# Kernel tuning notes

Hardware: AMD Instinct MI355X
Metric: run time of the kernel (lower is better)

Reference implementation:

```python
import jax, jax.numpy as jnp
import numpy as np

E = 1024        # embedding_dim
H = 16          # n_heads
DK = 64         # qk_dim
DV = 64         # v_dim
P = 512         # projection_dim (latent kv bottleneck)
BASE = 10000.0


def rope(x):
    # x: [B, H, S, D] with D even; interleaved (even/odd) RoPE rotation
    S, D = x.shape[-2], x.shape[-1]
    theta = BASE ** (-2.0 * jnp.arange(D // 2, dtype=x.dtype) / D)      # [D/2]
    ang = jnp.arange(S, dtype=x.dtype)[:, None] * theta[None, :]        # [S, D/2]
    cos, sin = jnp.cos(ang), jnp.sin(ang)
    x1, x2 = x[..., ::2], x[..., 1::2]                                  # [B,H,S,D/2]
    out = jnp.stack([x1 * cos - x2 * sin, x1 * sin + x2 * cos], axis=-1)
    return out.reshape(x.shape)


def setup_inputs() -> dict:
    key = jax.random.key(0)
    ks = jax.random.split(key, 10)
    s = lambda fan_in: 1.0 / np.sqrt(fan_in)
    x = jax.random.normal(ks[0], (2, 2048, E), dtype=jnp.float32)
    Wq = jax.random.uniform(ks[1], (E, DK * H), jnp.float32, -s(E), s(E))
    bq = jax.random.uniform(ks[2], (DK * H,), jnp.float32, -s(E), s(E))
    Wkv1 = jax.random.uniform(ks[3], (E, P), jnp.float32, -s(E), s(E))
    bkv1 = jax.random.uniform(ks[4], (P,), jnp.float32, -s(E), s(E))
    Wkv2 = jax.random.uniform(ks[5], (P, (DK + DV) * H), jnp.float32, -s(P), s(P))
    bkv2 = jax.random.uniform(ks[6], ((DK + DV) * H,), jnp.float32, -s(P), s(P))
    Wo = jax.random.uniform(ks[7], (H * DV, E), jnp.float32, -s(H * DV), s(H * DV))
    bo = jax.random.uniform(ks[8], (E,), jnp.float32, -s(H * DV), s(H * DV))
    return {"x": x, "Wq": Wq, "bq": bq, "Wkv1": Wkv1, "bkv1": bkv1,
            "Wkv2": Wkv2, "bkv2": bkv2, "Wo": Wo, "bo": bo}


def reference(x, Wq, bq, Wkv1, bkv1, Wkv2, bkv2, Wo, bo):
    B, S, _ = x.shape  # seq == max_context, so truncation x[:, -max_context:] is a no-op
    q = x @ Wq + bq                                            # [B,S,H*DK]
    kv = (x @ Wkv1 + bkv1) @ Wkv2 + bkv2                       # [B,S,(DK+DV)*H]
    k, v = kv[..., : DK * H], kv[..., DK * H:]
    q = q.reshape(B, S, H, DK).transpose(0, 2, 1, 3)           # [B,H,S,DK]
    k = k.reshape(B, S, H, DK).transpose(0, 2, 1, 3)
    v = v.reshape(B, S, H, DV).transpose(0, 2, 1, 3)           # [B,H,S,DV]
    q = rope(q)
    k = rope(k)
    scores = jnp.einsum('bhqd,bhkd->bhqk', q, k) * (1.0 / np.sqrt(DK))
    causal = jnp.tril(jnp.ones((S, S), dtype=bool))
    scores = jnp.where(causal, scores, -jnp.inf)
    probs = jax.nn.softmax(scores, axis=-1)                    # dropout skipped (eval)
    attn = jnp.einsum('bhqk,bhkd->bhqd', probs, v)             # [B,H,S,DV]
    attn = attn.transpose(0, 2, 1, 3).reshape(B, S, H * DV)
    return attn @ Wo + bo                                      # [B,S,E]
```

## Files before the change

### kernel.cpp

```cpp
#include <hip/hip_runtime.h>
#include <hip/hip_bf16.h>
#include <stdint.h>
#include <math.h>

#define S_ 2048
#define H_ 16
#define B_ 2

typedef __attribute__((ext_vector_type(4))) float f32x4;
typedef __attribute__((ext_vector_type(8))) short s16x8;

static __device__ __forceinline__ uint16_t f2bf(float f) {
    union { float f; uint32_t u; } x; x.f = f;
    uint32_t u = x.u;
    return (uint16_t)((u + 0x7FFFu + ((u >> 16) & 1u)) >> 16);
}

static __device__ __forceinline__ void gl_lds16(const uint16_t* g, uint16_t* l) {
    __builtin_amdgcn_global_load_lds(
        (const __attribute__((address_space(1))) unsigned int*)g,
        (__attribute__((address_space(3))) unsigned int*)l, 16, 0, 0);
}


__global__ void cvt_f32_bf16(const float* __restrict__ in, uint16_t* __restrict__ out, int n4) {
    int i = blockIdx.x * blockDim.x + threadIdx.x;
    if (i >= n4) return;
    float4 v = ((const float4*)in)[i];
    union { uint16_t h[4]; uint64_t q; } pk;
    pk.h[0] = f2bf(v.x); pk.h[1] = f2bf(v.y); pk.h[2] = f2bf(v.z); pk.h[3] = f2bf(v.w);
    ((uint64_t*)out)[i] = pk.q;
}

__global__ void transpose_w(const float* __restrict__ in, uint16_t* __restrict__ out, int R, int C) {
    __shared__ float sm[32][33];
    int r0 = blockIdx.x * 32, c0 = blockIdx.y * 32;
    int t = threadIdx.x;
    int rr = t >> 3, cc = (t & 7) * 4;
    float4 v = *(const float4*)(in + (size_t)(r0 + rr) * C + c0 + cc);
    sm[rr][cc] = v.x; sm[rr][cc + 1] = v.y; sm[rr][cc + 2] = v.z; sm[rr][cc + 3] = v.w;
    __syncthreads();
    union { uint16_t h[4]; uint64_t q; } pk;
    #pragma unroll
    for (int i = 0; i < 4; i++) pk.h[i] = f2bf(sm[cc + i][rr]);
    *(uint64_t*)(out + (size_t)(c0 + rr) * R + r0 + cc) = pk.q;
}

__global__ void rope_table(float* __restrict__ cosT, float* __restrict__ sinT) {
    int i = blockIdx.x * blockDim.x + threadIdx.x;
    int s = i >> 5, j = i & 31;
    float theta = powf(10000.0f, -2.0f * (float)j / 64.0f);
    float ang = (float)s * theta;
    cosT[i] = cosf(ang);
    sinT[i] = sinf(ang);
}

__global__ void vtrans(const uint16_t* __restrict__ vb, uint16_t* __restrict__ vt) {
    __shared__ __align__(16) uint16_t sm[64][72];
    int s0 = blockIdx.x * 64;
    int bh = blockIdx.y;
    const uint16_t* src = vb + (size_t)bh * S_ * 64;
    uint16_t* dst = vt + (size_t)bh * 64 * S_;
    int t = threadIdx.x;
    #pragma unroll
    for (int p = 0; p < 2; p++) {
        int off = p * 2048 + t * 8;
        int sl = off >> 6, d = off & 63;
        s16x8 v = *(const s16x8*)(src + (size_t)(s0 + sl) * 64 + d);
        #pragma unroll
        for (int i = 0; i < 8; i++) sm[sl][d + i] = (uint16_t)v[i];
    }
    __syncthreads();
    #pragma unroll
    for (int p = 0; p < 2; p++) {
        int off = p * 2048 + t * 8;
        int d = off >> 6, sl = off & 63;
        union { uint16_t h[8]; s16x8 v; } pk;
        #pragma unroll
        for (int i = 0; i < 8; i++) pk.h[i] = sm[sl + i][d];
        *(s16x8*)(dst + (size_t)d * S_ + s0 + sl) = pk.v;
    }
}


#define MODE_F32   0
#define MODE_BF16  1
#define MODE_QROPE 2
#define MODE_KV    3

#define QSCALE 0.180336880f

template<int MODE>
__global__ __launch_bounds__(256, 2)
void gemm_bt(const uint16_t* __restrict__ A, const uint16_t* __restrict__ BT,
             const float* __restrict__ bias,
             void* __restrict__ out0, uint16_t* __restrict__ out2,
             const float* __restrict__ cosT, const float* __restrict__ sinT,
             int N, int K)
{
    __shared__ __align__(16) uint16_t smA[128 * 32];
    __shared__ __align__(16) uint16_t smB[128 * 32];
    const int t = threadIdx.x;
    const int l = t & 63;
    const int wid = t >> 6;
    const int wr = wid >> 1, wc = wid & 1;
    const int m0 = blockIdx.x * 128, n0 = blockIdx.y * 128;

    f32x4 acc[4][4];
    #pragma unroll
    for (int i = 0; i < 4; i++)
        #pragma unroll
        for (int j = 0; j < 4; j++) acc[i][j] = (f32x4)(0.0f);

    const int srow = t >> 2;
    const int ssw = (((t & 3) ^ (srow & 3)) * 8);
    const uint16_t* aG = A + (size_t)(m0 + srow) * K + ssw;
    const uint16_t* bG = BT + (size_t)(n0 + srow) * K + ssw;
    uint16_t* lA = smA + t * 8;
    uint16_t* lB = smB + t * 8;

    const int rchunk = (((l >> 4) ^ (l & 3)) * 8);

    for (int k0 = 0; k0 < K; k0 += 32) {
        __syncthreads();
        gl_lds16(aG + k0, lA);
        gl_lds16(aG + (size_t)64 * K + k0, lA + 2048);
        gl_lds16(bG + k0, lB);
        gl_lds16(bG + (size_t)64 * K + k0, lB + 2048);
        __syncthreads();
        s16x8 af[4], bfr[4];
        #pragma unroll
        for (int mf = 0; mf < 4; mf++)
            af[mf] = *(const s16x8*)(smA + (wr * 64 + mf * 16 + (l & 15)) * 32 + rchunk);
        #pragma unroll
        for (int nf = 0; nf < 4; nf++)
            bfr[nf] = *(const s16x8*)(smB + (wc * 64 + nf * 16 + (l & 15)) * 32 + rchunk);
        #pragma unroll
        for (int mf = 0; mf < 4; mf++)
            #pragma unroll
            for (int nf = 0; nf < 4; nf++)
                acc[mf][nf] = __builtin_amdgcn_mfma_f32_16x16x32_bf16(af[mf], bfr[nf], acc[mf][nf], 0, 0, 0);
    }

    const int rbase = m0 + wr * 64 + ((l >> 4) << 2);
    const int cbase = n0 + wc * 64 + (l & 15);
    #pragma unroll
    for (int mf = 0; mf < 4; mf++) {
        #pragma unroll
        for (int nf = 0; nf < 4; nf++) {
            const int col = cbase + nf * 16;
            const float bv = bias[col];
            #pragma unroll
            for (int r = 0; r < 4; r++) {
                const int row = rbase + mf * 16 + r;
                float v = acc[mf][nf][r] + bv;
                if constexpr (MODE == MODE_F32) {
                    ((float*)out0)[(size_t)row * N + col] = v;
                } else if constexpr (MODE == MODE_BF16) {
                    ((uint16_t*)out0)[(size_t)row * N + col] = f2bf(v);
                } else {
                    float other = __shfl_xor(v, 1);
                    int s = row & (S_ - 1);
                    int b = row >> 11;
                    if constexpr (MODE == MODE_QROPE) {
                        int h = col >> 6, d = col & 63;
                        float c = cosT[s * 32 + (d >> 1)];
                        float sn = sinT[s * 32 + (d >> 1)];
                        float o = (d & 1) ? (other * sn + v * c) : (v * c - other * sn);
                        o *= QSCALE;
                        ((uint16_t*)out0)[((size_t)(b * H_ + h) * S_ + s) * 64 + d] = f2bf(o);
                    } else {
                        if (col < 1024) {
                            int h = col >> 6, d = col & 63;
                            float c = cosT[s * 32 + (d >> 1)];
                            float sn = sinT[s * 32 + (d >> 1)];
                            float o = (d & 1) ? (other * sn + v * c) : (v * c - other * sn);
                            ((uint16_t*)out0)[((size_t)(b * H_ + h) * S_ + s) * 64 + d] = f2bf(o);
                        } else {
                            int cc = col - 1024;
                            int h = cc >> 6, d = cc & 63;
                            out2[((size_t)(b * H_ + h) * S_ + s) * 64 + d] = f2bf(v);
                        }
                    }
                }
            }
        }
    }
}


__global__ __launch_bounds__(256, 4)
void attn_fa(const uint16_t* __restrict__ qr, const uint16_t* __restrict__ kr,
             const uint16_t* __restrict__ vt, uint16_t* __restrict__ attnf)
{
    __shared__ __align__(16) uint16_t smK[2][4096];
    __shared__ __align__(16) uint16_t smV[2][4096];
    __shared__ __align__(16) uint16_t smP[4096];

    const int t = threadIdx.x;
    const int l = t & 63;
    const int w = t >> 6;
    const int bh = blockIdx.y;
    const int bb = bh >> 4, hh = bh & 15;
    const uint16_t* qB = qr + (size_t)bh * S_ * 64;
    const uint16_t* kB = kr + (size_t)bh * S_ * 64;
    const uint16_t* vB = vt + (size_t)bh * 64 * S_;

    const int arow = t >> 3;
    const int asw = (((t & 7) ^ (arow & 7)) * 8);
    const int frow = l & 15;
    const int fg = l >> 4;
    const int rsw = l & 7;

    auto stage = [&](int buf, int kv0) {
        gl_lds16(kB + (size_t)(kv0 + arow) * 64 + asw, &smK[buf][t * 8]);
        gl_lds16(kB + (size_t)(kv0 + arow + 32) * 64 + asw, &smK[buf][2048 + t * 8]);
        gl_lds16(vB + (size_t)arow * S_ + kv0 + asw, &smV[buf][t * 8]);
        gl_lds16(vB + (size_t)(arow + 32) * S_ + kv0 + asw, &smV[buf][2048 + t * 8]);
    };

    auto process = [&](int qt) {
        s16x8 qf[2];
        {
            const uint16_t* qp = qB + (size_t)(qt * 64 + w * 16 + frow) * 64 + fg * 8;
            qf[0] = *(const s16x8*)qp;
            qf[1] = *(const s16x8*)(qp + 32);
        }
        float mrow[4], lrow[4];
        f32x4 oacc[4];
        #pragma unroll
        for (int r = 0; r < 4; r++) { mrow[r] = -INFINITY; lrow[r] = 0.0f; }
        #pragma unroll
        for (int nf = 0; nf < 4; nf++) oacc[nf] = (f32x4)(0.0f);

        const int nkt = qt + 1;
        int cur = 0;
        stage(0, qt ? 0 : 0);
        __syncthreads();

        for (int kt = 0; kt < nkt; kt++) {
            if (kt + 1 < nkt) stage(cur ^ 1, (kt + 1) * 64);

            f32x4 sacc[4];
            #pragma unroll
            for (int nf = 0; nf < 4; nf++) sacc[nf] = (f32x4)(0.0f);
            #pragma unroll
            for (int kk = 0; kk < 2; kk++) {
                #pragma unroll
                for (int nf = 0; nf < 4; nf++) {
                    s16x8 kf = *(const s16x8*)(&smK[cur][(nf * 16 + frow) * 64 + (((kk * 4 + fg) ^ rsw) * 8)]);
                    sacc[nf] = __builtin_amdgcn_mfma_f32_16x16x32_bf16(qf[kk], kf, sacc[nf], 0, 0, 0);
                }
            }

            const bool diag = (kt == qt);
            #pragma unroll
            for (int r = 0; r < 4; r++) {
                const int qloc = w * 16 + fg * 4 + r;
                float sv[4];
                #pragma unroll
                for (int nf = 0; nf < 4; nf++) {
                    float s = sacc[nf][r];
                    if (diag) s = (nf * 16 + frow <= qloc) ? s : -INFINITY;
                    sv[nf] = s;
                }
                float mx = fmaxf(fmaxf(sv[0], sv[1]), fmaxf(sv[2], sv[3]));
                mx = fmaxf(mx, __shfl_xor(mx, 1));
                mx = fmaxf(mx, __shfl_xor(mx, 2));
                mx = fmaxf(mx, __shfl_xor(mx, 4));
                mx = fmaxf(mx, __shfl_xor(mx, 8));
                float nm = fmaxf(mrow[r], mx);
                float fac = __builtin_amdgcn_exp2f(mrow[r] - nm);
                float ps = 0.0f;
                float pb[4];
                #pragma unroll
                for (int nf = 0; nf < 4; nf++) {
                    float p = __builtin_amdgcn_exp2f(sv[nf] - nm);
                    pb[nf] = p;
                    ps += p;
                }
                ps += __shfl_xor(ps, 1);
                ps += __shfl_xor(ps, 2);
                ps += __shfl_xor(ps, 4);
                ps += __shfl_xor(ps, 8);
                lrow[r] = lrow[r] * fac + ps;
                mrow[r] = nm;
                #pragma unroll
                for (int nf = 0; nf < 4; nf++) oacc[nf][r] *= fac;
                const int prow = w * 16 + fg * 4 + r;
                const int prm = (fg * 4 + r) & 7;
                #pragma unroll
                for (int nf = 0; nf < 4; nf++)
                    smP[prow * 64 + (((nf * 2 + (frow >> 3)) ^ prm) * 8) + (frow & 7)] = f2bf(pb[nf]);
            }

            #pragma unroll
            for (int kk = 0; kk < 2; kk++) {
                s16x8 pf = *(const s16x8*)(&smP[(w * 16 + frow) * 64 + (((kk * 4 + fg) ^ rsw) * 8)]);
                #pragma unroll
                for (int nf = 0; nf < 4; nf++) {
                    s16x8 vf = *(const s16x8*)(&smV[cur][(nf * 16 + frow) * 64 + (((kk * 4 + fg) ^ rsw) * 8)]);
                    oacc[nf] = __builtin_amdgcn_mfma_f32_16x16x32_bf16(pf, vf, oacc[nf], 0, 0, 0);
                }
            }

            __syncthreads();
            cur ^= 1;
        }

        #pragma unroll
        for (int r = 0; r < 4; r++) {
            float rinv = __builtin_amdgcn_rcpf(lrow[r]);
            const int qrow = qt * 64 + w * 16 + fg * 4 + r;
            #pragma unroll
            for (int nf = 0; nf < 4; nf++) {
                int d = nf * 16 + frow;
                attnf[((size_t)(bb * S_ + qrow)) * 1024 + hh * 64 + d] = f2bf(oacc[nf][r] * rinv);
            }
        }
    };

    const int j = blockIdx.x;
    process(j);
    process(31 - j);
}


extern "C" void kernel_launch(void* const* d_in, const int* in_sizes, int n_in,
                              void* d_out, int out_size, void* d_ws, size_t ws_size,
                              hipStream_t stream)
{
    const float* x    = (const float*)d_in[0];
    const float* Wq   = (const float*)d_in[1];
    const float* bq   = (const float*)d_in[2];
    const float* Wkv1 = (const float*)d_in[3];
    const float* bkv1 = (const float*)d_in[4];
    const float* Wkv2 = (const float*)d_in[5];
    const float* bkv2 = (const float*)d_in[6];
    const float* Wo   = (const float*)d_in[7];
    const float* bo   = (const float*)d_in[8];
    float* out = (float*)d_out;
    char* ws = (char*)d_ws;

    uint16_t* xb    = (uint16_t*)(ws + 0);
    uint16_t* WqT   = (uint16_t*)(ws + 8388608);
    uint16_t* Wkv1T = (uint16_t*)(ws + 10485760);
    uint16_t* Wkv2T = (uint16_t*)(ws + 11534336);
    uint16_t* WoT   = (uint16_t*)(ws + 13631488);
    float*    cosT  = (float*)(ws + 15728640);
    float*    sinT  = (float*)(ws + 15990784);
    uint16_t* qrb   = (uint16_t*)(ws + 16252928);
    uint16_t* kv1b  = (uint16_t*)(ws + 24641536);
    uint16_t* krb   = (uint16_t*)(ws + 28835840);
    uint16_t* vbb   = (uint16_t*)(ws + 37224448);
    uint16_t* vtb   = (uint16_t*)(ws + 45613056);
    uint16_t* attnf = (uint16_t*)(ws + 54001664);

    cvt_f32_bf16<<<4096, 256, 0, stream>>>(x, xb, 1048576);
    transpose_w<<<dim3(32, 32), 256, 0, stream>>>(Wq, WqT, 1024, 1024);
    transpose_w<<<dim3(32, 16), 256, 0, stream>>>(Wkv1, Wkv1T, 1024, 512);
    transpose_w<<<dim3(16, 64), 256, 0, stream>>>(Wkv2, Wkv2T, 512, 2048);
    transpose_w<<<dim3(32, 32), 256, 0, stream>>>(Wo, WoT, 1024, 1024);
    rope_table<<<256, 256, 0, stream>>>(cosT, sinT);

    gemm_bt<MODE_QROPE><<<dim3(32, 8), 256, 0, stream>>>(xb, WqT, bq, qrb, nullptr, cosT, sinT, 1024, 1024);
    gemm_bt<MODE_BF16><<<dim3(32, 4), 256, 0, stream>>>(xb, Wkv1T, bkv1, kv1b, nullptr, nullptr, nullptr, 512, 1024);
    gemm_bt<MODE_KV><<<dim3(32, 16), 256, 0, stream>>>(kv1b, Wkv2T, bkv2, krb, vbb, cosT, sinT, 2048, 512);
    vtrans<<<dim3(32, 32), 256, 0, stream>>>(vbb, vtb);
    attn_fa<<<dim3(16, 32), 256, 0, stream>>>(qrb, krb, vtb, attnf);
    gemm_bt<MODE_F32><<<dim3(32, 8), 256, 0, stream>>>(attnf, WoT, bo, out, nullptr, nullptr, nullptr, 1024, 1024);
}
```

Before: 275.5 us.

## Double-buffer GEMM with narrower tiles and restructure flash attention to transposed scores

The GEMM now uses 128x64 tiles with double-buffered LDS staging, one barrier per k-step and a higher occupancy target, and the launch grids are doubled to match. The attention kernel computes S^T (K as the A operand), so each lane owns a single query column and the row max and sum need only two cross-lane shuffles. P is packed with v_cvt_pk_bf16 into vector LDS stores, and one q-tile per block replaces the paired tiles. This is meant to cut barrier stalls and softmax shuffle overhead, at the risk of load imbalance across causal q-tiles and extra A reloads in the GEMM. The rope table now uses exp2f in place of powf.

```diff
diff --git a/kernel.cpp b/kernel.cpp
--- a/kernel.cpp
+++ b/kernel.cpp
@@ -14,6 +14,12 @@
     union { float f; uint32_t u; } x; x.f = f;
     uint32_t u = x.u;
     return (uint16_t)((u + 0x7FFFu + ((u >> 16) & 1u)) >> 16);
+}
+
+static __device__ __forceinline__ uint32_t cvtpk_bf16(float a, float b) {
+    uint32_t d;
+    asm("v_cvt_pk_bf16_f32 %0, %1, %2" : "=v"(d) : "v"(a), "v"(b));
+    return d;
 }
 
 static __device__ __forceinline__ void gl_lds16(const uint16_t* g, uint16_t* l) {
@@ -49,7 +55,7 @@
 __global__ void rope_table(float* __restrict__ cosT, float* __restrict__ sinT) {
     int i = blockIdx.x * blockDim.x + threadIdx.x;
     int s = i >> 5, j = i & 31;
-    float theta = powf(10000.0f, -2.0f * (float)j / 64.0f);
+    float theta = exp2f(-0.41524101f * (float)j);
     float ang = (float)s * theta;
     cosT[i] = cosf(ang);
     sinT[i] = sinf(ang);
@@ -91,63 +97,67 @@
 #define QSCALE 0.180336880f
 
 template<int MODE>
-__global__ __launch_bounds__(256, 2)
+__global__ __launch_bounds__(256, 4)
 void gemm_bt(const uint16_t* __restrict__ A, const uint16_t* __restrict__ BT,
              const float* __restrict__ bias,
              void* __restrict__ out0, uint16_t* __restrict__ out2,
              const float* __restrict__ cosT, const float* __restrict__ sinT,
              int N, int K)
 {
-    __shared__ __align__(16) uint16_t smA[128 * 32];
-    __shared__ __align__(16) uint16_t smB[128 * 32];
+    __shared__ __align__(16) uint16_t smA[2][4096];
+    __shared__ __align__(16) uint16_t smB[2][2048];
     const int t = threadIdx.x;
     const int l = t & 63;
     const int wid = t >> 6;
     const int wr = wid >> 1, wc = wid & 1;
-    const int m0 = blockIdx.x * 128, n0 = blockIdx.y * 128;
-
-    f32x4 acc[4][4];
+    const int m0 = blockIdx.x * 128, n0 = blockIdx.y * 64;
+
+    f32x4 acc[4][2];
     #pragma unroll
     for (int i = 0; i < 4; i++)
         #pragma unroll
-        for (int j = 0; j < 4; j++) acc[i][j] = (f32x4)(0.0f);
+        for (int j = 0; j < 2; j++) acc[i][j] = (f32x4)(0.0f);
 
     const int srow = t >> 2;
     const int ssw = (((t & 3) ^ (srow & 3)) * 8);
     const uint16_t* aG = A + (size_t)(m0 + srow) * K + ssw;
     const uint16_t* bG = BT + (size_t)(n0 + srow) * K + ssw;
-    uint16_t* lA = smA + t * 8;
-    uint16_t* lB = smB + t * 8;
 
     const int rchunk = (((l >> 4) ^ (l & 3)) * 8);
 
+    auto stage = [&](int buf, int k0) {
+        gl_lds16(aG + k0, &smA[buf][t * 8]);
+        gl_lds16(aG + (size_t)64 * K + k0, &smA[buf][2048 + t * 8]);
+        gl_lds16(bG + k0, &smB[buf][t * 8]);
+    };
+
+    stage(0, 0);
+    __syncthreads();
+    int cur = 0;
     for (int k0 = 0; k0 < K; k0 += 32) {
+        if (k0 + 32 < K) stage(cur ^ 1, k0 + 32);
+        s16x8 af[4], bfr[2];
+        #pragma unroll
+        for (int mf = 0; mf < 4; mf++)
+            af[mf] = *(const s16x8*)(&smA[cur][(wr * 64 + mf * 16 + (l & 15)) * 32 + rchunk]);
+        #pragma unroll
+        for (int nf = 0; nf < 2; nf++)
+            bfr[nf] = *(const s16x8*)(&smB[cur][(wc * 32 + nf * 16 + (l & 15)) * 32 + rchunk]);
+        #pragma unroll
+        for (int mf = 0; mf < 4; mf++)
+            #pragma unroll
+            for (int nf = 0; nf < 2; nf++)
+                acc[mf][nf] = __builtin_amdgcn_mfma_f32_16x16x32_bf16(af[mf], bfr[nf], acc[mf][nf], 0, 0, 0);
         __syncthreads();
-        gl_lds16(aG + k0, lA);
-        gl_lds16(aG + (size_t)64 * K + k0, lA + 2048);
-        gl_lds16(bG + k0, lB);
-        gl_lds16(bG + (size_t)64 * K + k0, lB + 2048);
-        __syncthreads();
-        s16x8 af[4], bfr[4];
-        #pragma unroll
-        for (int mf = 0; mf < 4; mf++)
-            af[mf] = *(const s16x8*)(smA + (wr * 64 + mf * 16 + (l & 15)) * 32 + rchunk);
-        #pragma unroll
-        for (int nf = 0; nf < 4; nf++)
-            bfr[nf] = *(const s16x8*)(smB + (wc * 64 + nf * 16 + (l & 15)) * 32 + rchunk);
-        #pragma unroll
-        for (int mf = 0; mf < 4; mf++)
-            #pragma unroll
-            for (int nf = 0; nf < 4; nf++)
-                acc[mf][nf] = __builtin_amdgcn_mfma_f32_16x16x32_bf16(af[mf], bfr[nf], acc[mf][nf], 0, 0, 0);
+        cur ^= 1;
     }
 
     const int rbase = m0 + wr * 64 + ((l >> 4) << 2);
-    const int cbase = n0 + wc * 64 + (l & 15);
+    const int cbase = n0 + wc * 32 + (l & 15);
     #pragma unroll
     for (int mf = 0; mf < 4; mf++) {
         #pragma unroll
-        for (int nf = 0; nf < 4; nf++) {
+        for (int nf = 0; nf < 2; nf++) {
             const int col = cbase + nf * 16;
             const float bv = bias[col];
             #pragma unroll
@@ -210,7 +220,10 @@
     const int asw = (((t & 7) ^ (arow & 7)) * 8);
     const int frow = l & 15;
     const int fg = l >> 4;
-    const int rsw = l & 7;
+    const int rsw = frow & 7;
+
+    const int qt = 31 - blockIdx.x;
+    const int qglob = qt * 64 + w * 16 + frow;
 
     auto stage = [&](int buf, int kv0) {
         gl_lds16(kB + (size_t)(kv0 + arow) * 64 + asw, &smK[buf][t * 8]);
@@ -219,110 +232,109 @@
         gl_lds16(vB + (size_t)(arow + 32) * S_ + kv0 + asw, &smV[buf][2048 + t * 8]);
     };
 
-    auto process = [&](int qt) {
-        s16x8 qf[2];
-        {
-            const uint16_t* qp = qB + (size_t)(qt * 64 + w * 16 + frow) * 64 + fg * 8;
-            qf[0] = *(const s16x8*)qp;
-            qf[1] = *(const s16x8*)(qp + 32);
-        }
-        float mrow[4], lrow[4];
-        f32x4 oacc[4];
-        #pragma unroll
-        for (int r = 0; r < 4; r++) { mrow[r] = -INFINITY; lrow[r] = 0.0f; }
-        #pragma unroll
-        for (int nf = 0; nf < 4; nf++) oacc[nf] = (f32x4)(0.0f);
-
-        const int nkt = qt + 1;
-        int cur = 0;
-        stage(0, qt ? 0 : 0);
+    s16x8 qf[2];
+    {
+        const uint16_t* qp = qB + (size_t)qglob * 64 + fg * 8;
+        qf[0] = *(const s16x8*)qp;
+        qf[1] = *(const s16x8*)(qp + 32);
+    }
+
+    float mreg = -INFINITY, lsum = 0.0f;
+    f32x4 oacc[4];
+    #pragma unroll
+    for (int nf = 0; nf < 4; nf++) oacc[nf] = (f32x4)(0.0f);
+
+    stage(0, 0);
+    __syncthreads();
+    int cur = 0;
+    const int wfr = w * 16 + frow;
+
+    for (int kt = 0; kt <= qt; kt++) {
+        if (kt < qt) stage(cur ^ 1, (kt + 1) * 64);
+
+        f32x4 sacc[4];
+        #pragma unroll
+        for (int nf = 0; nf < 4; nf++) sacc[nf] = (f32x4)(0.0f);
+        #pragma unroll
+        for (int kk = 0; kk < 2; kk++) {
+            #pragma unroll
+            for (int nf = 0; nf < 4; nf++) {
+                s16x8 kf = *(const s16x8*)(&smK[cur][(nf * 16 + frow) * 64 + (((kk * 4 + fg) ^ rsw) * 8)]);
+                sacc[nf] = __builtin_amdgcn_mfma_f32_16x16x32_bf16(kf, qf[kk], sacc[nf], 0, 0, 0);
+            }
+        }
+
+        if (kt == qt) {
+            #pragma unroll
+            for (int nf = 0; nf < 4; nf++)
+                #pragma unroll
+                for (int r = 0; r < 4; r++)
+                    sacc[nf][r] = (nf * 16 + fg * 4 + r <= wfr) ? sacc[nf][r] : -INFINITY;
+        }
+        float mx = -INFINITY;
+        #pragma unroll
+        for (int nf = 0; nf < 4; nf++)
+            #pragma unroll
+            for (int r = 0; r < 4; r++) mx = fmaxf(mx, sacc[nf][r]);
+        mx = fmaxf(mx, __shfl_xor(mx, 16));
+        mx = fmaxf(mx, __shfl_xor(mx, 32));
+        float nm = fmaxf(mreg, mx);
+        float fac = __builtin_amdgcn_exp2f(mreg - nm);
+        mreg = nm;
+        float ps = 0.0f;
+        #pragma unroll
+        for (int nf = 0; nf < 4; nf++)
+            #pragma unroll
+            for (int r = 0; r < 4; r++) {
+                float p = __builtin_amdgcn_exp2f(sacc[nf][r] - nm);
+                sacc[nf][r] = p;
+                ps += p;
+            }
+        ps += __shfl_xor(ps, 16);
+        ps += __shfl_xor(ps, 32);
+        lsum = lsum * fac + ps;
+
+        #pragma unroll
+        for (int nf = 0; nf < 4; nf++) {
+            uint32_t w0 = cvtpk_bf16(sacc[nf][0], sacc[nf][1]);
+            uint32_t w1 = cvtpk_bf16(sacc[nf][2], sacc[nf][3]);
+            int chunk = (nf * 2 + (fg >> 1)) ^ rsw;
+            uint2 pkd; pkd.x = w0; pkd.y = w1;
+            *(uint2*)(&smP[(w * 16 + frow) * 64 + chunk * 8 + (fg & 1) * 4]) = pkd;
+        }
+
+        #pragma unroll
+        for (int r = 0; r < 4; r++) {
+            float facr = __shfl(fac, fg * 16 + fg * 4 + r);
+            #pragma unroll
+            for (int nf = 0; nf < 4; nf++) oacc[nf][r] *= facr;
+        }
+
+        #pragma unroll
+        for (int kk = 0; kk < 2; kk++) {
+            s16x8 pf = *(const s16x8*)(&smP[(w * 16 + frow) * 64 + (((kk * 4 + fg) ^ rsw) * 8)]);
+            #pragma unroll
+            for (int nf = 0; nf < 4; nf++) {
+                s16x8 vf = *(const s16x8*)(&smV[cur][(nf * 16 + frow) * 64 + (((kk * 4 + fg) ^ rsw) * 8)]);
+                oacc[nf] = __builtin_amdgcn_mfma_f32_16x16x32_bf16(pf, vf, oacc[nf], 0, 0, 0);
+            }
+        }
+
         __syncthreads();
-
-        for (int kt = 0; kt < nkt; kt++) {
-            if (kt + 1 < nkt) stage(cur ^ 1, (kt + 1) * 64);
-
-            f32x4 sacc[4];
-            #pragma unroll
-            for (int nf = 0; nf < 4; nf++) sacc[nf] = (f32x4)(0.0f);
-            #pragma unroll
-            for (int kk = 0; kk < 2; kk++) {
-                #pragma unroll
-                for (int nf = 0; nf < 4; nf++) {
-                    s16x8 kf = *(const s16x8*)(&smK[cur][(nf * 16 + frow) * 64 + (((kk * 4 + fg) ^ rsw) * 8)]);
-                    sacc[nf] = __builtin_amdgcn_mfma_f32_16x16x32_bf16(qf[kk], kf, sacc[nf], 0, 0, 0);
-                }
-            }
-
-            const bool diag = (kt == qt);
-            #pragma unroll
-            for (int r = 0; r < 4; r++) {
-                const int qloc = w * 16 + fg * 4 + r;
-                float sv[4];
-                #pragma unroll
-                for (int nf = 0; nf < 4; nf++) {
-                    float s = sacc[nf][r];
-                    if (diag) s = (nf * 16 + frow <= qloc) ? s : -INFINITY;
-                    sv[nf] = s;
-                }
-                float mx = fmaxf(fmaxf(sv[0], sv[1]), fmaxf(sv[2], sv[3]));
-                mx = fmaxf(mx, __shfl_xor(mx, 1));
-                mx = fmaxf(mx, __shfl_xor(mx, 2));
-                mx = fmaxf(mx, __shfl_xor(mx, 4));
-                mx = fmaxf(mx, __shfl_xor(mx, 8));
-                float nm = fmaxf(mrow[r], mx);
-                float fac = __builtin_amdgcn_exp2f(mrow[r] - nm);
-                float ps = 0.0f;
-                float pb[4];
-                #pragma unroll
-                for (int nf = 0; nf < 4; nf++) {
-                    float p = __builtin_amdgcn_exp2f(sv[nf] - nm);
-                    pb[nf] = p;
-                    ps += p;
-                }
-                ps += __shfl_xor(ps, 1);
-                ps += __shfl_xor(ps, 2);
-                ps += __shfl_xor(ps, 4);
-                ps += __shfl_xor(ps, 8);
-                lrow[r] = lrow[r] * fac + ps;
-                mrow[r] = nm;
-                #pragma unroll
-                for (int nf = 0; nf < 4; nf++) oacc[nf][r] *= fac;
-                const int prow = w * 16 + fg * 4 + r;
-                const int prm = (fg * 4 + r) & 7;
-                #pragma unroll
-                for (int nf = 0; nf < 4; nf++)
-                    smP[prow * 64 + (((nf * 2 + (frow >> 3)) ^ prm) * 8) + (frow & 7)] = f2bf(pb[nf]);
-            }
-
-            #pragma unroll
-            for (int kk = 0; kk < 2; kk++) {
-                s16x8 pf = *(const s16x8*)(&smP[(w * 16 + frow) * 64 + (((kk * 4 + fg) ^ rsw) * 8)]);
-                #pragma unroll
-                for (int nf = 0; nf < 4; nf++) {
-                    s16x8 vf = *(const s16x8*)(&smV[cur][(nf * 16 + frow) * 64 + (((kk * 4 + fg) ^ rsw) * 8)]);
-                    oacc[nf] = __builtin_amdgcn_mfma_f32_16x16x32_bf16(pf, vf, oacc[nf], 0, 0, 0);
-                }
-            }
-
-            __syncthreads();
-            cur ^= 1;
-        }
-
-        #pragma unroll
-        for (int r = 0; r < 4; r++) {
-            float rinv = __builtin_amdgcn_rcpf(lrow[r]);
-            const int qrow = qt * 64 + w * 16 + fg * 4 + r;
-            #pragma unroll
-            for (int nf = 0; nf < 4; nf++) {
-                int d = nf * 16 + frow;
-                attnf[((size_t)(bb * S_ + qrow)) * 1024 + hh * 64 + d] = f2bf(oacc[nf][r] * rinv);
-            }
-        }
-    };
-
-    const int j = blockIdx.x;
-    process(j);
-    process(31 - j);
+        cur ^= 1;
+    }
+
+    #pragma unroll
+    for (int r = 0; r < 4; r++) {
+        float lr = __shfl(lsum, fg * 16 + fg * 4 + r);
+        float rinv = __builtin_amdgcn_rcpf(lr);
+        const int qrow = qt * 64 + w * 16 + fg * 4 + r;
+        #pragma unroll
+        for (int nf = 0; nf < 4; nf++) {
+            int d = nf * 16 + frow;
+            attnf[((size_t)(bb * S_ + qrow)) * 1024 + hh * 64 + d] = f2bf(oacc[nf][r] * rinv);
+        }
+    }
 }
 
 
@@ -363,10 +375,10 @@
     transpose_w<<<dim3(32, 32), 256, 0, stream>>>(Wo, WoT, 1024, 1024);
     rope_table<<<256, 256, 0, stream>>>(cosT, sinT);
 
-    gemm_bt<MODE_QROPE><<<dim3(32, 8), 256, 0, stream>>>(xb, WqT, bq, qrb, nullptr, cosT, sinT, 1024, 1024);
-    gemm_bt<MODE_BF16><<<dim3(32, 4), 256, 0, stream>>>(xb, Wkv1T, bkv1, kv1b, nullptr, nullptr, nullptr, 512, 1024);
-    gemm_bt<MODE_KV><<<dim3(32, 16), 256, 0, stream>>>(kv1b, Wkv2T, bkv2, krb, vbb, cosT, sinT, 2048, 512);
+    gemm_bt<MODE_QROPE><<<dim3(32, 16), 256, 0, stream>>>(xb, WqT, bq, qrb, nullptr, cosT, sinT, 1024, 1024);
+    gemm_bt<MODE_BF16><<<dim3(32, 8), 256, 0, stream>>>(xb, Wkv1T, bkv1, kv1b, nullptr, nullptr, nullptr, 512, 1024);
+    gemm_bt<MODE_KV><<<dim3(32, 32), 256, 0, stream>>>(kv1b, Wkv2T, bkv2, krb, vbb, cosT, sinT, 2048, 512);
     vtrans<<<dim3(32, 32), 256, 0, stream>>>(vbb, vtb);
-    attn_fa<<<dim3(16, 32), 256, 0, stream>>>(qrb, krb, vtb, attnf);
-    gemm_bt<MODE_F32><<<dim3(32, 8), 256, 0, stream>>>(attnf, WoT, bo, out, nullptr, nullptr, nullptr, 1024, 1024);
-}
+    attn_fa<<<dim3(32, 32), 256, 0, stream>>>(qrb, krb, vtb, attnf);
+    gemm_bt<MODE_F32><<<dim3(32, 16), 256, 0, stream>>>(attnf, WoT, bo, out, nullptr, nullptr, nullptr, 1024, 1024);
+}
```

Result: faster. 247.2 us (-10.3%).
